# Kernel tuning notes

Hardware: AMD Instinct MI355X
Metric: run time of the kernel (lower is better)

Reference implementation:

```python
import jax, jax.numpy as jnp
import numpy as np

N = 16384      # nodes
IN_DIM = 256   # input feature dim
H = 256        # hidden dim
K = 16         # kNN neighbors
L = 2          # GCN layers
C = 10         # classes


def setup_inputs() -> dict:
    key = jax.random.key(0)
    ks = jax.random.split(key, 9)
    s = 0.05
    return {
        "x": jax.random.normal(ks[0], (1, N, IN_DIM), jnp.float32),
        "W_pre": jax.random.normal(ks[1], (H, IN_DIM), jnp.float32) * s,
        "b_pre": jnp.zeros((H,), jnp.float32),
        "W_conv": jax.random.normal(ks[2], (L, H, H), jnp.float32) * s,
        "b_conv": jnp.zeros((L, H), jnp.float32),
        "W_fc1": jax.random.normal(ks[3], (H // 2, H), jnp.float32) * s,
        "b_fc1": jnp.zeros((H // 2,), jnp.float32),
        "W_fc2": jax.random.normal(ks[4], (C, H // 2), jnp.float32) * s,
        "b_fc2": jnp.zeros((C,), jnp.float32),
    }


def _knn_edges(h):
    # h: [N, H]. torch.cdist + topk(k+1, largest=False); squared dist preserves order.
    sq = jnp.sum(h * h, axis=-1)                      # [N]
    d2 = sq[:, None] + sq[None, :] - 2.0 * (h @ h.T)  # [N, N]
    _, idx = jax.lax.top_k(-d2, K + 1)                # smallest k+1
    idx = idx[:, 1:]                                  # drop self, [N, K]
    src = jnp.repeat(jnp.arange(N), K)
    dst = idx.reshape(-1)
    # bidirectional edges (cat with flipped), as in build_knn_graph
    s_idx = jnp.concatenate([src, dst])
    t_idx = jnp.concatenate([dst, src])
    return s_idx, t_idx


def _gcn_layer(h, W, b, s_idx, t_idx, norm):
    m = h @ W.T                                             # PyG GCNConv: lin then propagate
    out = jax.ops.segment_sum(m[s_idx] * norm[:, None], t_idx, num_segments=N)
    return out + b


def reference(x, W_pre, b_pre, W_conv, b_conv, W_fc1, b_fc1, W_fc2, b_fc2):
    # pre_fc (dropout inactive in eval)
    h = jax.nn.relu(x @ W_pre.T + b_pre)   # [1, N, H]
    h0 = h[0]                              # B=1
    s_idx, t_idx = _knn_edges(h0)
    # add self loops (GCNConv default)
    loop = jnp.arange(N)
    s_idx = jnp.concatenate([s_idx, loop])
    t_idx = jnp.concatenate([t_idx, loop])
    # symmetric normalization D^{-1/2} (A+I) D^{-1/2}
    deg = jax.ops.segment_sum(jnp.ones_like(s_idx, dtype=h0.dtype), t_idx, num_segments=N)
    dinv = jnp.where(deg > 0, jax.lax.rsqrt(deg), 0.0)
    norm = dinv[s_idx] * dinv[t_idx]
    hf = h0
    for l in range(L):
        hf = jax.nn.relu(_gcn_layer(hf, W_conv[l], b_conv[l], s_idx, t_idx, norm))
    hf = hf[None]                          # [1, N, H]
    hid = jax.nn.relu(hf @ W_fc1.T + b_fc1)
    pred = hid @ W_fc2.T + b_fc2           # [1, N, C]
    return pred
```

## Files before the change

### kernel.cpp

```cpp
#include <hip/hip_runtime.h>

#define NN   16384
#define DIM  256
#define KNN  16
#define SEG  8
#define JT_PER (NN / SEG / 128)

typedef __attribute__((ext_vector_type(8))) short  bf16x8;
typedef __attribute__((ext_vector_type(4))) float  f32x4;

__device__ __forceinline__ void gload_lds16b(const unsigned short* g, void* l)
{
    __builtin_amdgcn_global_load_lds(
        (const __attribute__((address_space(1))) unsigned int*)g,
        (__attribute__((address_space(3))) unsigned int*)l, 16, 0, 0);
}

__device__ __forceinline__ unsigned short f2bf(float x)
{
    unsigned int u = __float_as_uint(x);
    unsigned int r = (u + 0x7fffu + ((u >> 16) & 1u)) >> 16;
    return (unsigned short)r;
}

__device__ __forceinline__ unsigned pack_key(float d, int j)
{
    return (__float_as_uint(fmaxf(d, 0.0f)) & 0xFFFFC000u) | (unsigned)j;
}

__global__ __launch_bounds__(256)
void convert_bf16_k(const float* __restrict__ in, unsigned short* __restrict__ out)
{
    const int i4 = blockIdx.x * 256 + threadIdx.x;
    float4 v = *(const float4*)&in[(size_t)i4 * 4];
    ushort4 b;
    b.x = f2bf(v.x); b.y = f2bf(v.y); b.z = f2bf(v.z); b.w = f2bf(v.w);
    *(ushort4*)&out[(size_t)i4 * 4] = b;
}

template<bool RELU, bool BIAS, bool BF16OUT>
__global__ __launch_bounds__(256)
void gemm_nt(const float* __restrict__ A, const float* __restrict__ W,
             const float* __restrict__ bias,
             float* __restrict__ C, unsigned short* __restrict__ Cb,
             int M, int K, int NO)
{
    __shared__ __align__(16) float As[16][68];
    __shared__ __align__(16) float Ws[16][68];
    const int tid = threadIdx.x;
    const int tx = tid & 15, ty = tid >> 4;
    const int row0 = blockIdx.y * 64, col0 = blockIdx.x * 64;
    const int lr = tid >> 2;
    const int lk = (tid & 3) * 4;

    float acc[4][4] = {};

    for (int k0 = 0; k0 < K; k0 += 16) {
        float4 av = *(const float4*)&A[(size_t)(row0 + lr) * K + k0 + lk];
        float4 wv = *(const float4*)&W[(size_t)(col0 + lr) * K + k0 + lk];
        __syncthreads();
        As[lk+0][lr] = av.x; As[lk+1][lr] = av.y; As[lk+2][lr] = av.z; As[lk+3][lr] = av.w;
        Ws[lk+0][lr] = wv.x; Ws[lk+1][lr] = wv.y; Ws[lk+2][lr] = wv.z; Ws[lk+3][lr] = wv.w;
        __syncthreads();
        #pragma unroll
        for (int kk = 0; kk < 16; ++kk) {
            float4 a = *(const float4*)&As[kk][ty*4];
            float4 b = *(const float4*)&Ws[kk][tx*4];
            acc[0][0] += a.x*b.x; acc[0][1] += a.x*b.y; acc[0][2] += a.x*b.z; acc[0][3] += a.x*b.w;
            acc[1][0] += a.y*b.x; acc[1][1] += a.y*b.y; acc[1][2] += a.y*b.z; acc[1][3] += a.y*b.w;
            acc[2][0] += a.z*b.x; acc[2][1] += a.z*b.y; acc[2][2] += a.z*b.z; acc[2][3] += a.z*b.w;
            acc[3][0] += a.w*b.x; acc[3][1] += a.w*b.y; acc[3][2] += a.w*b.z; acc[3][3] += a.w*b.w;
        }
    }

    #pragma unroll
    for (int rr = 0; rr < 4; ++rr) {
        const int r = row0 + ty*4 + rr;
        float o[4];
        #pragma unroll
        for (int cc = 0; cc < 4; ++cc) {
            float v = acc[rr][cc];
            if (BIAS) v += bias[col0 + tx*4 + cc];
            if (RELU) v = fmaxf(v, 0.0f);
            o[cc] = v;
        }
        *(float4*)&C[(size_t)r * NO + col0 + tx*4] = make_float4(o[0], o[1], o[2], o[3]);
        if (BF16OUT) {
            ushort4 bv;
            bv.x = f2bf(o[0]); bv.y = f2bf(o[1]);
            bv.z = f2bf(o[2]); bv.w = f2bf(o[3]);
            *(ushort4*)&Cb[(size_t)r * NO + col0 + tx*4] = bv;
        }
    }
}

template<bool RELU, bool BIAS, bool ROWSCALE, bool F32OUT>
__global__ __launch_bounds__(256, 1)
void gemm_mfma(const unsigned short* __restrict__ Ab, const unsigned short* __restrict__ Wb,
               const float* __restrict__ bias, const float* __restrict__ rscale,
               float* __restrict__ C, unsigned short* __restrict__ Cb, int NO)
{
    __shared__ __align__(16) float smem[25088];
    unsigned short* stA = (unsigned short*)smem;
    unsigned short* stB = (unsigned short*)(smem + 4096);
    float* D = smem + 8192;

    const int tid  = threadIdx.x;
    const int lane = tid & 63;
    const int wave = tid >> 6;
    const int wj = wave >> 1;
    const int wi = wave & 1;
    const int l15 = lane & 15;
    const int g   = lane >> 4;
    const int R0 = blockIdx.y * 128;
    const int C0 = blockIdx.x * 128;

    f32x4 acc[4][4];
    #pragma unroll
    for (int fa = 0; fa < 4; ++fa)
        #pragma unroll
        for (int fb = 0; fb < 4; ++fb)
            acc[fa][fb] = (f32x4){0.f, 0.f, 0.f, 0.f};

    #pragma unroll 1
    for (int ch = 0; ch < 4; ++ch) {
        const int k0g = ch * 64;
        __syncthreads();
        #pragma unroll
        for (int it = 0; it < 4; ++it) {
            const int lin = tid + it * 256;
            const int row = lin >> 3, f = lin & 7;
            const int kq = f ^ (row & 7);
            gload_lds16b(&Ab[(size_t)(R0 + row) * 256 + k0g + kq * 8],
                         (char*)stA + lin * 16);
            gload_lds16b(&Wb[(size_t)(C0 + row) * 256 + k0g + kq * 8],
                         (char*)stB + lin * 16);
        }
        __syncthreads();

        #pragma unroll
        for (int k0 = 0; k0 < 64; k0 += 32) {
            const int ub = (k0 >> 3) + g;
            bf16x8 af[4], bf[4];
            #pragma unroll
            for (int fb = 0; fb < 4; ++fb) {
                const int jr = wj*64 + fb*16 + l15;
                const int ir = wi*64 + fb*16 + l15;
                af[fb] = *(const bf16x8*)((char*)stB + jr*128 + ((ub ^ (jr & 7)) * 16));
                bf[fb] = *(const bf16x8*)((char*)stA + ir*128 + ((ub ^ (ir & 7)) * 16));
            }
            #pragma unroll
            for (int fa = 0; fa < 4; ++fa)
                #pragma unroll
                for (int fb = 0; fb < 4; ++fb)
                    acc[fa][fb] = __builtin_amdgcn_mfma_f32_16x16x32_bf16(
                        af[fa], bf[fb], acc[fa][fb], 0, 0, 0);
        }
    }

    #pragma unroll
    for (int fa = 0; fa < 4; ++fa)
        #pragma unroll
        for (int fb = 0; fb < 4; ++fb) {
            const int i_ = wi*64 + fb*16 + l15;
            const int j0 = wj*64 + fa*16 + g*4;
            *(f32x4*)&D[i_ * 132 + j0] = acc[fa][fb];
        }
    __syncthreads();

    #pragma unroll
    for (int it = 0; it < 16; ++it) {
        const int linear = it * 256 + tid;
        const int r = linear >> 5, c4 = linear & 31;
        float4 v = *(const float4*)&D[r * 132 + c4 * 4];
        const float s = ROWSCALE ? rscale[R0 + r] : 1.0f;
        float o[4] = {v.x * s, v.y * s, v.z * s, v.w * s};
        #pragma unroll
        for (int cc = 0; cc < 4; ++cc) {
            if (BIAS) o[cc] += bias[C0 + c4*4 + cc];
            if (RELU) o[cc] = fmaxf(o[cc], 0.0f);
        }
        if (F32OUT) {
            *(float4*)&C[(size_t)(R0 + r) * NO + C0 + c4*4] =
                make_float4(o[0], o[1], o[2], o[3]);
        } else {
            ushort4 bv;
            bv.x = f2bf(o[0]); bv.y = f2bf(o[1]);
            bv.z = f2bf(o[2]); bv.w = f2bf(o[3]);
            *(ushort4*)&Cb[(size_t)(R0 + r) * NO + C0 + c4*4] = bv;
        }
    }
}

__global__ __launch_bounds__(256)
void sq_kernel(const float* __restrict__ h0, float* __restrict__ sq)
{
    const int wid = threadIdx.x >> 6, lane = threadIdx.x & 63;
    const int row = blockIdx.x * 4 + wid;
    float4 v = *(const float4*)&h0[(size_t)row * DIM + lane * 4];
    float s = v.x*v.x + v.y*v.y + v.z*v.z + v.w*v.w;
    #pragma unroll
    for (int o = 32; o > 0; o >>= 1) s += __shfl_down(s, o);
    if (lane == 0) sq[row] = s;
}

__device__ __forceinline__ void key_insert(unsigned (&kl)[16], unsigned k)
{
    #pragma unroll
    for (int p = 0; p < 16; ++p) {
        const unsigned lo = min(kl[p], k);
        k = max(kl[p], k);
        kl[p] = lo;
    }
}

__global__ __launch_bounds__(256, 3)
void knn_topk(const unsigned short* __restrict__ h0b, const float* __restrict__ sq,
              unsigned* __restrict__ cand)
{
    __shared__ __align__(16) float smem[8704];
    char* sbase = (char*)smem;
    unsigned short* stA = (unsigned short*)sbase;
    unsigned short* stB = (unsigned short*)(sbase + 16384);
    float* D = smem;

    const int tid  = threadIdx.x;
    const int lane = tid & 63;
    const int wave = tid >> 6;
    const int wj = wave >> 1;
    const int wi = wave & 1;
    const int l15 = lane & 15;
    const int g   = lane >> 4;
    const int R0 = blockIdx.y * 128;
    const int seg = blockIdx.x;

    const int orow  = tid >> 1;
    const int ohalf = tid & 1;
    const int myrow = R0 + orow;
    const float osq = sq[myrow];

    unsigned kl[16];
    #pragma unroll
    for (int e = 0; e < 16; ++e) kl[e] = 0xFFFFFFFFu;

    for (int jt = 0; jt < JT_PER; ++jt) {
        const int C0 = seg * (NN / SEG) + jt * 128;
        const bool diag = (C0 == R0);
        f32x4 acc[4][4];
        #pragma unroll
        for (int fa = 0; fa < 4; ++fa)
            #pragma unroll
            for (int fb = 0; fb < 4; ++fb)
                acc[fa][fb] = (f32x4){0.f, 0.f, 0.f, 0.f};

        #pragma unroll 1
        for (int ch = 0; ch < 4; ++ch) {
            const int k0g = ch * 64;
            __syncthreads();
            #pragma unroll
            for (int it = 0; it < 4; ++it) {
                const int lin = tid + it * 256;
                const int row = lin >> 3, f = lin & 7;
                const int kq = f ^ (row & 7);
                gload_lds16b(&h0b[(size_t)(R0 + row) * DIM + k0g + kq * 8],
                             (char*)stA + lin * 16);
                gload_lds16b(&h0b[(size_t)(C0 + row) * DIM + k0g + kq * 8],
                             (char*)stB + lin * 16);
            }
            __syncthreads();

            #pragma unroll
            for (int k0 = 0; k0 < 64; k0 += 32) {
                const int ub = (k0 >> 3) + g;
                bf16x8 af[4], bf[4];
                #pragma unroll
                for (int fb = 0; fb < 4; ++fb) {
                    const int jr = wj*64 + fb*16 + l15;
                    const int ir = wi*64 + fb*16 + l15;
                    af[fb] = *(const bf16x8*)((char*)stB + jr*128 + ((ub ^ (jr & 7)) * 16));
                    bf[fb] = *(const bf16x8*)((char*)stA + ir*128 + ((ub ^ (ir & 7)) * 16));
                }
                #pragma unroll
                for (int fa = 0; fa < 4; ++fa)
                    #pragma unroll
                    for (int fb = 0; fb < 4; ++fb)
                        acc[fa][fb] = __builtin_amdgcn_mfma_f32_16x16x32_bf16(
                            af[fa], bf[fb], acc[fa][fb], 0, 0, 0);
            }
        }

        #pragma unroll 1
        for (int h = 0; h < 2; ++h) {
            __syncthreads();
            if (wj == h) {
                #pragma unroll
                for (int fa = 0; fa < 4; ++fa)
                    #pragma unroll
                    for (int fb = 0; fb < 4; ++fb) {
                        const int i_ = wi*64 + fb*16 + l15;
                        *(f32x4*)&D[i_ * 68 + fa*16 + g*4] = acc[fa][fb];
                    }
            }
            __syncthreads();

            const int cb = C0 + h*64 + ohalf*32;
            const float* Dr = &D[orow * 68 + ohalf * 32];
            #pragma clang loop unroll(disable)
            for (int e = 0; e < 8; ++e) {
                const float4 dv4 = *(const float4*)&Dr[e * 4];
                const float4 sv4 = *(const float4*)&sq[cb + e * 4];
                const int j0 = cb + e * 4;
                unsigned k0 = pack_key((osq + sv4.x) - 2.0f * dv4.x, j0 + 0);
                unsigned k1 = pack_key((osq + sv4.y) - 2.0f * dv4.y, j0 + 1);
                unsigned k2 = pack_key((osq + sv4.z) - 2.0f * dv4.z, j0 + 2);
                unsigned k3 = pack_key((osq + sv4.w) - 2.0f * dv4.w, j0 + 3);
                if (diag) {
                    if (j0 + 0 == myrow) k0 = 0xFFFFFFFFu;
                    if (j0 + 1 == myrow) k1 = 0xFFFFFFFFu;
                    if (j0 + 2 == myrow) k2 = 0xFFFFFFFFu;
                    if (j0 + 3 == myrow) k3 = 0xFFFFFFFFu;
                }
                const unsigned kmin = min(min(k0, k1), min(k2, k3));
                if (kmin < kl[15]) {
                    if (k0 < kl[15]) key_insert(kl, k0);
                    if (k1 < kl[15]) key_insert(kl, k1);
                    if (k2 < kl[15]) key_insert(kl, k2);
                    if (k3 < kl[15]) key_insert(kl, k3);
                }
            }
        }
    }

    __syncthreads();
    unsigned* ck = (unsigned*)smem;
    #pragma unroll
    for (int e = 0; e < 16; ++e) ck[tid * 17 + e] = kl[e];
    __syncthreads();
    if (tid < 128) {
        const unsigned* LA = &ck[(2*tid) * 17];
        const unsigned* LB = &ck[(2*tid + 1) * 17];
        int pa = 0, pb = 0;
        const size_t obase = ((size_t)seg * NN + R0 + tid) * 16;
        #pragma clang loop unroll(disable)
        for (int r = 0; r < 16; ++r) {
            const unsigned ka = LA[pa], kb = LB[pb];
            const bool takeA = (ka < kb);
            cand[obase + r] = takeA ? ka : kb;
            if (takeA) ++pa; else ++pb;
        }
    }
}

__global__ __launch_bounds__(256)
void merge32_k(const unsigned* __restrict__ cand, int* __restrict__ cand32)
{
    const int tid = threadIdx.x;
    const int row = blockIdx.x * 32 + (tid >> 3);
    const int l = tid & 7;
    int head = 0;
    for (int r = 0; r < 32; ++r) {
        const size_t base = ((size_t)l * NN + row) * 16;
        unsigned mk = (head < 16) ? cand[base + head] : 0xFFFFFFFFu;
        int ml = l;
        #pragma unroll
        for (int off = 1; off < 8; off <<= 1) {
            const unsigned ok = __shfl_xor(mk, off);
            const int      ol = __shfl_xor(ml, off);
            if (ok < mk) { mk = ok; ml = ol; }
        }
        if (ml == l) ++head;
        if (l == 0) cand32[(size_t)row * 32 + r] = (int)(mk & 0x3FFFu);
    }
}

__global__ __launch_bounds__(256)
void refine_k(const float* __restrict__ h0, const float* __restrict__ sq,
              const int* __restrict__ cand32, int* __restrict__ nbr)
{
    const int tid = threadIdx.x;
    const int sub = tid & 31;
    const int row = blockIdx.x * 8 + (tid >> 5);
    const int j = cand32[(size_t)row * 32 + sub];
    float dot = 0.0f;
    #pragma clang loop unroll_count(4)
    for (int k = 0; k < DIM; k += 4) {
        float4 a = *(const float4*)&h0[(size_t)row * DIM + k];
        float4 b = *(const float4*)&h0[(size_t)j * DIM + k];
        dot += a.x*b.x + a.y*b.y + a.z*b.z + a.w*b.w;
    }
    float d = sq[row] + sq[j] - 2.0f * dot;
    const int ji = j;
    for (int t = 0; t < 16; ++t) {
        float md = d; int mi = ji;
        #pragma unroll
        for (int off = 1; off < 32; off <<= 1) {
            const float od = __shfl_xor(md, off);
            const int   oi = __shfl_xor(mi, off);
            if (od < md || (od == md && oi < mi)) { md = od; mi = oi; }
        }
        if (d == md && ji == mi) d = 3e38f;
        if (sub == 0) nbr[(size_t)row * KNN + t] = mi;
    }
}

__global__ void count_k(const int* __restrict__ nbr, int* __restrict__ indeg)
{
    const int e = blockIdx.x * 256 + threadIdx.x;
    atomicAdd(&indeg[nbr[e]], 1);
}

__global__ __launch_bounds__(1024)
void scan_k(const int* __restrict__ indeg, int* __restrict__ offs,
            float* __restrict__ dinv)
{
    __shared__ int part[1024];
    const int t = threadIdx.x;
    int pre[16]; int s = 0;
    #pragma unroll
    for (int j = 0; j < 16; ++j) { pre[j] = s; s += indeg[t*16 + j]; }
    part[t] = s;
    __syncthreads();
    for (int d = 1; d < 1024; d <<= 1) {
        int v = (t >= d) ? part[t - d] : 0;
        __syncthreads();
        part[t] += v;
        __syncthreads();
    }
    const int base = (t > 0) ? part[t-1] : 0;
    #pragma unroll
    for (int j = 0; j < 16; ++j) {
        offs[t*16 + j] = base + pre[j];
        dinv[t*16 + j] = rsqrtf((float)(indeg[t*16 + j] + KNN + 1));
    }
}

__global__ void fill_k(const int* __restrict__ nbr, const int* __restrict__ offs,
                       int* __restrict__ cursor, int* __restrict__ rev)
{
    const int e = blockIdx.x * 256 + threadIdx.x;
    const int v = nbr[e];
    const int i = e >> 4;
    const int p = atomicAdd(&cursor[v], 1);
    rev[offs[v] + p] = i;
}

__device__ __forceinline__ void acc_row8(float (&acc)[8], const unsigned short* p)
{
    const uint4 u = *(const uint4*)p;
    acc[0] += __uint_as_float(u.x << 16);
    acc[1] += __uint_as_float(u.x & 0xffff0000u);
    acc[2] += __uint_as_float(u.y << 16);
    acc[3] += __uint_as_float(u.y & 0xffff0000u);
    acc[4] += __uint_as_float(u.z << 16);
    acc[5] += __uint_as_float(u.z & 0xffff0000u);
    acc[6] += __uint_as_float(u.w << 16);
    acc[7] += __uint_as_float(u.w & 0xffff0000u);
}

__global__ __launch_bounds__(256)
void gatherv_k(const unsigned short* __restrict__ mb, const int* __restrict__ nbr,
               const int* __restrict__ rev, const int* __restrict__ offs,
               const int* __restrict__ indeg, const float* __restrict__ dinv,
               const float* __restrict__ bias, unsigned short* __restrict__ outb)
{
    __shared__ float red[8][256];
    const int v   = blockIdx.x;
    const int tid = threadIdx.x;
    const int grp = tid >> 5;
    const int sub = tid & 31;
    const int f0  = sub * 8;

    float acc[8] = {};
    #pragma clang loop unroll(disable)
    for (int t = grp; t < 17; t += 8) {
        const int u = (t == 16) ? v : nbr[(size_t)v * KNN + t];
        acc_row8(acc, &mb[(size_t)u * DIM + f0]);
    }
    const int o = offs[v], n = indeg[v];
    #pragma clang loop unroll_count(2)
    for (int t = grp; t < n; t += 8) {
        acc_row8(acc, &mb[(size_t)rev[o + t] * DIM + f0]);
    }

    #pragma unroll
    for (int e = 0; e < 8; ++e) red[grp][f0 + e] = acc[e];
    __syncthreads();

    float s = 0.0f;
    #pragma unroll
    for (int g2 = 0; g2 < 8; ++g2) s += red[g2][tid];
    const float r = dinv[v] * s + bias[tid];
    outb[(size_t)v * DIM + tid] = f2bf(fmaxf(r, 0.0f));
}

__global__ __launch_bounds__(256)
void fc2_k(const float* __restrict__ hid, const float* __restrict__ W,
           const float* __restrict__ b, float* __restrict__ out)
{
    __shared__ float Ws[1280];
    __shared__ float bs[16];
    const int tid = threadIdx.x;
    for (int i = tid; i < 1280; i += 256) Ws[i] = W[i];
    if (tid < 10) bs[tid] = b[tid];
    __syncthreads();
    const int row = blockIdx.x * 8 + (tid >> 5);
    const int sub = tid & 31;
    float4 h4 = *(const float4*)&hid[(size_t)row * 128 + sub * 4];
    float a[10];
    #pragma unroll
    for (int c = 0; c < 10; ++c) {
        float4 w4 = *(const float4*)&Ws[c * 128 + sub * 4];
        a[c] = h4.x*w4.x + h4.y*w4.y + h4.z*w4.z + h4.w*w4.w;
    }
    #pragma unroll
    for (int off = 16; off >= 1; off >>= 1)
        #pragma unroll
        for (int c = 0; c < 10; ++c) a[c] += __shfl_down(a[c], off, 32);
    if (sub == 0) {
        #pragma unroll
        for (int c = 0; c < 10; ++c) out[(size_t)row * 10 + c] = a[c] + bs[c];
    }
}

extern "C" void kernel_launch(void* const* d_in, const int* in_sizes, int n_in,
                              void* d_out, int out_size, void* d_ws, size_t ws_size,
                              hipStream_t stream)
{
    const float* x     = (const float*)d_in[0];
    const float* Wpre  = (const float*)d_in[1];
    const float* bpre  = (const float*)d_in[2];
    const float* Wconv = (const float*)d_in[3];
    const float* bconv = (const float*)d_in[4];
    const float* Wfc1  = (const float*)d_in[5];
    const float* bfc1  = (const float*)d_in[6];
    const float* Wfc2  = (const float*)d_in[7];
    const float* bfc2  = (const float*)d_in[8];
    float* out = (float*)d_out;

    float* ws    = (float*)d_ws;
    float* h0    = ws;
    float* mbuf  = h0    + (size_t)NN*DIM;
    float* hfbuf = mbuf  + (size_t)NN*DIM;
    float* hid   = hfbuf + (size_t)NN*DIM;
    float* sqv   = hid   + (size_t)NN*128;
    float* dinv  = sqv   + NN;
    int*   nbr   = (int*)(dinv + NN);
    int*   indeg = nbr   + (size_t)NN*KNN;
    int*   offs  = indeg + NN;
    int*   cursor= offs  + NN;
    int*   rev   = cursor+ NN;
    unsigned short* wbc  = (unsigned short*)(rev + (size_t)NN*KNN);
    unsigned short* wbf1 = wbc + 2*256*256;

    unsigned short* h0b   = (unsigned short*)hid;
    unsigned* cand  = (unsigned*)hfbuf;
    int*   cand32 = (int*)mbuf;
    unsigned short* m1b   = (unsigned short*)mbuf;
    unsigned short* m2b   = (unsigned short*)h0;
    unsigned short* hf_b  = (unsigned short*)hfbuf;
    unsigned short* hf2_b = (unsigned short*)(hfbuf + (size_t)NN*DIM/2);

    hipMemsetAsync(indeg,  0, NN*sizeof(int), stream);
    hipMemsetAsync(cursor, 0, NN*sizeof(int), stream);

    convert_bf16_k<<<2*256*256/1024, 256, 0, stream>>>(Wconv, wbc);
    convert_bf16_k<<<128*256/1024,   256, 0, stream>>>(Wfc1, wbf1);

    gemm_nt<true,true,true><<<dim3(DIM/64, NN/64), 256, 0, stream>>>(
        x, Wpre, bpre, h0, h0b, NN, DIM, DIM);
    sq_kernel<<<NN/4, 256, 0, stream>>>(h0, sqv);
    knn_topk<<<dim3(SEG, NN/128), 256, 0, stream>>>(h0b, sqv, cand);
    merge32_k<<<NN/32, 256, 0, stream>>>(cand, cand32);
    refine_k<<<NN/8, 256, 0, stream>>>(h0, sqv, cand32, nbr);
    count_k<<<NN*KNN/256, 256, 0, stream>>>(nbr, indeg);
    scan_k<<<1, 1024, 0, stream>>>(indeg, offs, dinv);
    fill_k<<<NN*KNN/256, 256, 0, stream>>>(nbr, offs, cursor, rev);
    gemm_mfma<false,false,true,false><<<dim3(DIM/128, NN/128), 256, 0, stream>>>(
        h0b, wbc, nullptr, dinv, nullptr, m1b, DIM);
    gatherv_k<<<NN, 256, 0, stream>>>(m1b, nbr, rev, offs, indeg, dinv, bconv, hf_b);
    gemm_mfma<false,false,true,false><<<dim3(DIM/128, NN/128), 256, 0, stream>>>(
        hf_b, wbc + 256*256, nullptr, dinv, nullptr, m2b, DIM);
    gatherv_k<<<NN, 256, 0, stream>>>(m2b, nbr, rev, offs, indeg, dinv, bconv + DIM, hf2_b);
    gemm_mfma<true,true,false,true><<<dim3(128/128, NN/128), 256, 0, stream>>>(
        hf2_b, wbf1, bfc1, nullptr, hid, nullptr, 128);
    fc2_k<<<NN/8, 256, 0, stream>>>(hid, Wfc2, bfc2, out);
}
```

Measured before the change: 827.6 us.

## Replace FP32 pre-FC SIMT GEMM with split-bf16 3-pass MFMA GEMM

Replaces the scalar FP32 tiled GEMM for the pre_fc layer with an MFMA-based kernel. Inputs and weights are first split into bf16 hi and lo parts, and three bf16 MFMA products (hi*lo, lo*hi, hi*hi) approximate FP32 accuracy, which keeps the kNN graph stable. This moves the pre-FC compute onto matrix cores. The cost is two extra conversion kernels and the extra traffic of writing and reading the hi/lo copies of x.

```diff
diff --git a/kernel.cpp b/kernel.cpp
--- a/kernel.cpp
+++ b/kernel.cpp
@@ -22,6 +22,10 @@
     unsigned int r = (u + 0x7fffu + ((u >> 16) & 1u)) >> 16;
     return (unsigned short)r;
 }
+__device__ __forceinline__ float bf2f(unsigned short u)
+{
+    return __uint_as_float(((unsigned)u) << 16);
+}
 
 __device__ __forceinline__ unsigned pack_key(float d, int j)
 {
@@ -38,59 +42,124 @@
     *(ushort4*)&out[(size_t)i4 * 4] = b;
 }
 
-template<bool RELU, bool BIAS, bool BF16OUT>
 __global__ __launch_bounds__(256)
-void gemm_nt(const float* __restrict__ A, const float* __restrict__ W,
-             const float* __restrict__ bias,
-             float* __restrict__ C, unsigned short* __restrict__ Cb,
-             int M, int K, int NO)
-{
-    __shared__ __align__(16) float As[16][68];
-    __shared__ __align__(16) float Ws[16][68];
-    const int tid = threadIdx.x;
-    const int tx = tid & 15, ty = tid >> 4;
-    const int row0 = blockIdx.y * 64, col0 = blockIdx.x * 64;
-    const int lr = tid >> 2;
-    const int lk = (tid & 3) * 4;
-
-    float acc[4][4] = {};
-
-    for (int k0 = 0; k0 < K; k0 += 16) {
-        float4 av = *(const float4*)&A[(size_t)(row0 + lr) * K + k0 + lk];
-        float4 wv = *(const float4*)&W[(size_t)(col0 + lr) * K + k0 + lk];
+void convert_hilo_k(const float* __restrict__ in,
+                    unsigned short* __restrict__ hi, unsigned short* __restrict__ lo)
+{
+    const int i4 = blockIdx.x * 256 + threadIdx.x;
+    float4 v = *(const float4*)&in[(size_t)i4 * 4];
+    ushort4 h, l;
+    h.x = f2bf(v.x); l.x = f2bf(v.x - bf2f(h.x));
+    h.y = f2bf(v.y); l.y = f2bf(v.y - bf2f(h.y));
+    h.z = f2bf(v.z); l.z = f2bf(v.z - bf2f(h.z));
+    h.w = f2bf(v.w); l.w = f2bf(v.w - bf2f(h.w));
+    *(ushort4*)&hi[(size_t)i4 * 4] = h;
+    *(ushort4*)&lo[(size_t)i4 * 4] = l;
+}
+
+__global__ __launch_bounds__(256, 1)
+void pre_mfma(const unsigned short* __restrict__ xh, const unsigned short* __restrict__ xl,
+              const unsigned short* __restrict__ wh, const unsigned short* __restrict__ wl,
+              const float* __restrict__ bias,
+              float* __restrict__ C, unsigned short* __restrict__ Cb)
+{
+    __shared__ __align__(16) float smem[16896];
+    unsigned short* stAh = (unsigned short*)smem;
+    unsigned short* stAl = (unsigned short*)((char*)smem + 16384);
+    unsigned short* stBh = (unsigned short*)((char*)smem + 32768);
+    unsigned short* stBl = (unsigned short*)((char*)smem + 49152);
+    float* D = smem;
+
+    const int tid  = threadIdx.x;
+    const int lane = tid & 63;
+    const int wave = tid >> 6;
+    const int wj = wave >> 1;
+    const int wi = wave & 1;
+    const int l15 = lane & 15;
+    const int g   = lane >> 4;
+    const int R0 = blockIdx.y * 128;
+    const int C0 = blockIdx.x * 128;
+
+    f32x4 acc[4][4];
+    #pragma unroll
+    for (int fa = 0; fa < 4; ++fa)
+        #pragma unroll
+        for (int fb = 0; fb < 4; ++fb)
+            acc[fa][fb] = (f32x4){0.f, 0.f, 0.f, 0.f};
+
+    #pragma unroll 1
+    for (int ch = 0; ch < 4; ++ch) {
+        const int k0g = ch * 64;
         __syncthreads();
-        As[lk+0][lr] = av.x; As[lk+1][lr] = av.y; As[lk+2][lr] = av.z; As[lk+3][lr] = av.w;
-        Ws[lk+0][lr] = wv.x; Ws[lk+1][lr] = wv.y; Ws[lk+2][lr] = wv.z; Ws[lk+3][lr] = wv.w;
+        #pragma unroll
+        for (int it = 0; it < 4; ++it) {
+            const int lin = tid + it * 256;
+            const int row = lin >> 3, f = lin & 7;
+            const int kq = f ^ (row & 7);
+            gload_lds16b(&xh[(size_t)(R0 + row) * 256 + k0g + kq * 8], (char*)stAh + lin * 16);
+            gload_lds16b(&xl[(size_t)(R0 + row) * 256 + k0g + kq * 8], (char*)stAl + lin * 16);
+            gload_lds16b(&wh[(size_t)(C0 + row) * 256 + k0g + kq * 8], (char*)stBh + lin * 16);
+            gload_lds16b(&wl[(size_t)(C0 + row) * 256 + k0g + kq * 8], (char*)stBl + lin * 16);
+        }
         __syncthreads();
-        #pragma unroll
-        for (int kk = 0; kk < 16; ++kk) {
-            float4 a = *(const float4*)&As[kk][ty*4];
-            float4 b = *(const float4*)&Ws[kk][tx*4];
-            acc[0][0] += a.x*b.x; acc[0][1] += a.x*b.y; acc[0][2] += a.x*b.z; acc[0][3] += a.x*b.w;
-            acc[1][0] += a.y*b.x; acc[1][1] += a.y*b.y; acc[1][2] += a.y*b.z; acc[1][3] += a.y*b.w;
-            acc[2][0] += a.z*b.x; acc[2][1] += a.z*b.y; acc[2][2] += a.z*b.z; acc[2][3] += a.z*b.w;
-            acc[3][0] += a.w*b.x; acc[3][1] += a.w*b.y; acc[3][2] += a.w*b.z; acc[3][3] += a.w*b.w;
-        }
-    }
-
-    #pragma unroll
-    for (int rr = 0; rr < 4; ++rr) {
-        const int r = row0 + ty*4 + rr;
-        float o[4];
+
+        #pragma unroll
+        for (int k0 = 0; k0 < 64; k0 += 32) {
+            const int ub = (k0 >> 3) + g;
+            bf16x8 afh[4], afl[4], bfh[4], bfl[4];
+            #pragma unroll
+            for (int q = 0; q < 4; ++q) {
+                const int jr = wj*64 + q*16 + l15;
+                const int ir = wi*64 + q*16 + l15;
+                const int oj = (ub ^ (jr & 7)) * 16;
+                const int oi = (ub ^ (ir & 7)) * 16;
+                afh[q] = *(const bf16x8*)((char*)stBh + jr*128 + oj);
+                afl[q] = *(const bf16x8*)((char*)stBl + jr*128 + oj);
+                bfh[q] = *(const bf16x8*)((char*)stAh + ir*128 + oi);
+                bfl[q] = *(const bf16x8*)((char*)stAl + ir*128 + oi);
+            }
+            #pragma unroll
+            for (int fa = 0; fa < 4; ++fa)
+                #pragma unroll
+                for (int fb = 0; fb < 4; ++fb) {
+                    acc[fa][fb] = __builtin_amdgcn_mfma_f32_16x16x32_bf16(
+                        afh[fa], bfl[fb], acc[fa][fb], 0, 0, 0);
+                    acc[fa][fb] = __builtin_amdgcn_mfma_f32_16x16x32_bf16(
+                        afl[fa], bfh[fb], acc[fa][fb], 0, 0, 0);
+                    acc[fa][fb] = __builtin_amdgcn_mfma_f32_16x16x32_bf16(
+                        afh[fa], bfh[fb], acc[fa][fb], 0, 0, 0);
+                }
+        }
+    }
+
+    __syncthreads();
+    #pragma unroll
+    for (int fa = 0; fa < 4; ++fa)
+        #pragma unroll
+        for (int fb = 0; fb < 4; ++fb) {
+            const int i_ = wi*64 + fb*16 + l15;
+            const int j0 = wj*64 + fa*16 + g*4;
+            *(f32x4*)&D[i_ * 132 + j0] = acc[fa][fb];
+        }
+    __syncthreads();
+
+    #pragma unroll
+    for (int it = 0; it < 16; ++it) {
+        const int linear = it * 256 + tid;
+        const int r = linear >> 5, c4 = linear & 31;
+        float4 v = *(const float4*)&D[r * 132 + c4 * 4];
+        float o[4] = {v.x, v.y, v.z, v.w};
         #pragma unroll
         for (int cc = 0; cc < 4; ++cc) {
-            float v = acc[rr][cc];
-            if (BIAS) v += bias[col0 + tx*4 + cc];
-            if (RELU) v = fmaxf(v, 0.0f);
-            o[cc] = v;
-        }
-        *(float4*)&C[(size_t)r * NO + col0 + tx*4] = make_float4(o[0], o[1], o[2], o[3]);
-        if (BF16OUT) {
-            ushort4 bv;
-            bv.x = f2bf(o[0]); bv.y = f2bf(o[1]);
-            bv.z = f2bf(o[2]); bv.w = f2bf(o[3]);
-            *(ushort4*)&Cb[(size_t)r * NO + col0 + tx*4] = bv;
-        }
+            o[cc] += bias[C0 + c4*4 + cc];
+            o[cc] = fmaxf(o[cc], 0.0f);
+        }
+        *(float4*)&C[(size_t)(R0 + r) * 256 + C0 + c4*4] =
+            make_float4(o[0], o[1], o[2], o[3]);
+        ushort4 bv;
+        bv.x = f2bf(o[0]); bv.y = f2bf(o[1]);
+        bv.z = f2bf(o[2]); bv.w = f2bf(o[3]);
+        *(ushort4*)&Cb[(size_t)(R0 + r) * 256 + C0 + c4*4] = bv;
     }
 }
 
@@ -551,8 +620,12 @@
     int*   rev   = cursor+ NN;
     unsigned short* wbc  = (unsigned short*)(rev + (size_t)NN*KNN);
     unsigned short* wbf1 = wbc + 2*256*256;
+    unsigned short* wph  = wbf1 + 128*256;
+    unsigned short* wpl  = wph + 256*256;
 
     unsigned short* h0b   = (unsigned short*)hid;
+    unsigned short* xh    = (unsigned short*)mbuf;
+    unsigned short* xl    = xh + (size_t)NN*DIM;
     unsigned* cand  = (unsigned*)hfbuf;
     int*   cand32 = (int*)mbuf;
     unsigned short* m1b   = (unsigned short*)mbuf;
@@ -563,11 +636,13 @@
     hipMemsetAsync(indeg,  0, NN*sizeof(int), stream);
     hipMemsetAsync(cursor, 0, NN*sizeof(int), stream);
 
+    convert_hilo_k<<<NN*DIM/1024, 256, 0, stream>>>(x, xh, xl);
+    convert_hilo_k<<<DIM*DIM/1024, 256, 0, stream>>>(Wpre, wph, wpl);
     convert_bf16_k<<<2*256*256/1024, 256, 0, stream>>>(Wconv, wbc);
     convert_bf16_k<<<128*256/1024,   256, 0, stream>>>(Wfc1, wbf1);
 
-    gemm_nt<true,true,true><<<dim3(DIM/64, NN/64), 256, 0, stream>>>(
-        x, Wpre, bpre, h0, h0b, NN, DIM, DIM);
+    pre_mfma<<<dim3(DIM/128, NN/128), 256, 0, stream>>>(
+        xh, xl, wph, wpl, bpre, h0, h0b);
     sq_kernel<<<NN/4, 256, 0, stream>>>(h0, sqv);
     knn_topk<<<dim3(SEG, NN/128), 256, 0, stream>>>(h0b, sqv, cand);
     merge32_k<<<NN/32, 256, 0, stream>>>(cand, cand32);
```

Measured after the change: 819.6 us. Within noise of the previous version (-1.0%).
